# Optimization experiments

Hardware: AMD Instinct MI355X
Metric: run time of the kernel (lower is better)

Reference implementation:

```python
import jax, jax.numpy as jnp
import numpy as np

TEMPERATURE = 0.7
BIG_NEG = -1e30  # safe stand-in for -inf (keeps grads finite)


def setup_inputs() -> dict:
    key = jax.random.key(0)
    k1, k2, k3 = jax.random.split(key, 3)
    B, D = 8192, 256
    embeddings = jax.random.normal(k1, (B, D), dtype=jnp.float32)
    categories = jax.random.randint(k2, (B,), 0, 16, dtype=jnp.int64)
    font_labels = jax.random.randint(k3, (B,), 0, 2000, dtype=jnp.int64)
    return {"embeddings": embeddings, "categories": categories, "font_labels": font_labels}


def reference(embeddings, categories, font_labels):
    # L2-normalize rows
    e = embeddings / jnp.linalg.norm(embeddings, axis=1, keepdims=True)
    sims = jnp.matmul(e, e.T) / TEMPERATURE  # [B, B]
    B = sims.shape[0]

    same = categories[:, None] == categories[None, :]
    diag = jnp.eye(B, dtype=bool)
    pos_mask = same & ~diag           # same category, excluding self
    neg_mask = ~same                  # different category (self excluded implicitly)

    valid = pos_mask.any(axis=1) & neg_mask.any(axis=1)

    pos_sim = jnp.max(jnp.where(pos_mask, sims, BIG_NEG), axis=1)  # hardest positive per anchor
    neg_max = jnp.max(jnp.where(neg_mask, sims, BIG_NEG), axis=1)

    # logsumexp over {pos_sim} U neg_sims, numerically stable
    m = jnp.where(valid, jnp.maximum(pos_sim, neg_max), 0.0)
    pos_safe = jnp.where(valid, pos_sim, 0.0)
    exp_neg_sum = jnp.sum(jnp.where(neg_mask, jnp.exp(sims - m[:, None]), 0.0), axis=1)
    lse = m + jnp.log(jnp.exp(pos_safe - m) + exp_neg_sum)

    loss_per_anchor = -pos_safe + lse
    n_valid = jnp.maximum(jnp.sum(valid), 1)
    return jnp.sum(jnp.where(valid, loss_per_anchor, 0.0)) / n_valid
```

## Files before the change

kernel.cpp:

```cpp
#include <hip/hip_runtime.h>
#include <stdint.h>

#define NROWS 8192
#define DDIM 256
#define RB 128
#define NRB (NROWS / RB)
#define BN 32
#define NTILES (RB / BN)
#define NSLOT NRB

#define ESCALE 1.4356159f
#define LN2F   0.6931471806f
#define NEGBIG (-1e30f)

typedef __attribute__((ext_vector_type(8))) short short8;
typedef __attribute__((ext_vector_type(4))) float f32x4;

typedef __attribute__((address_space(3))) void lds_void;
typedef const __attribute__((address_space(1))) void gl_void;

__device__ __forceinline__ unsigned short f2bf(float x) {
  unsigned int u = __float_as_uint(x);
  u += 0x7fffu + ((u >> 16) & 1u);
  return (unsigned short)(u >> 16);
}

__global__ __launch_bounds__(256) void knorm(const float* __restrict__ emb,
                                             unsigned short* __restrict__ ebf) {
  const int wave = threadIdx.x >> 6, lane = threadIdx.x & 63;
  const int row = blockIdx.x * 4 + wave;
  const float4 v = *(const float4*)(emb + row * DDIM + lane * 4);
  float ss = v.x * v.x + v.y * v.y + v.z * v.z + v.w * v.w;
#pragma unroll
  for (int off = 1; off < 64; off <<= 1) ss += __shfl_xor(ss, off, 64);
  const float sc = rsqrtf(ss) * ESCALE;
  ushort4 o;
  o.x = f2bf(v.x * sc); o.y = f2bf(v.y * sc);
  o.z = f2bf(v.z * sc); o.w = f2bf(v.w * sc);
  *(ushort4*)(ebf + row * DDIM + lane * 4) = o;
}

__global__ __launch_bounds__(256) void kmain(const unsigned short* __restrict__ ebf,
                                             const int* __restrict__ cats,
                                             float* __restrict__ posP,
                                             float* __restrict__ sumP) {
  const int I = blockIdx.y, J = blockIdx.x;
  if (J < I) return;
  __shared__ alignas(16) unsigned short smem[2][BN * DDIM];
  __shared__ float cpm[4][RB], cns[4][RB];
  const int tid = threadIdx.x;
  const int lane = tid & 63, wave = tid >> 6;
  const int lane15 = lane & 15, quad = lane >> 4;
  const bool offd = (I != J);
  const int rowG = I * RB + wave * 32;
  const int col0 = J * RB;

  short8 a[2][8];
#pragma unroll
  for (int m = 0; m < 2; ++m)
#pragma unroll
    for (int kk = 0; kk < 8; ++kk)
      a[m][kk] = *(const short8*)(ebf + (rowG + m * 16 + lane15) * DDIM + kk * 32 + quad * 8);

  int cati[2][4];
#pragma unroll
  for (int m = 0; m < 2; ++m)
#pragma unroll
    for (int r = 0; r < 4; ++r)
      cati[m][r] = cats[rowG + m * 16 + quad * 4 + r];

  bool dlr[4];
#pragma unroll
  for (int r = 0; r < 4; ++r) dlr[r] = (lane15 == quad * 4 + r);

  float pm[2][4], ns[2][4];
#pragma unroll
  for (int m = 0; m < 2; ++m)
#pragma unroll
    for (int r = 0; r < 4; ++r) { pm[m][r] = NEGBIG; ns[m][r] = 0.f; }

#define STAGE(t, buf)                                                           \
  {                                                                             \
    const unsigned short* g = ebf +                                             \
        (size_t)(col0 + (t) * BN + (lane & 31)) * DDIM +                        \
        (wave * 2 + (lane >> 5)) * 8;                                           \
    char* lb = (char*)&smem[(buf)][0] + wave * 1024;                            \
    _Pragma("unroll")                                                           \
    for (int c = 0; c < 4; ++c)                                                 \
      __builtin_amdgcn_global_load_lds((gl_void*)(g + c * 64),                  \
                                       (lds_void*)(lb + c * 4096), 16, 0, 0);   \
  }

  STAGE(0, 0);

  for (int t = 0; t < NTILES; ++t) {
    __syncthreads();
    if (t + 1 < NTILES) STAGE(t + 1, (t + 1) & 1);
    const char* bb = (const char*)&smem[t & 1][0];
    const int colBase = col0 + t * BN;
    const int cjt[2] = {cats[colBase + lane15], cats[colBase + 16 + lane15]};

#pragma unroll
    for (int nt = 0; nt < 2; ++nt) {
      short8 b[8];
#pragma unroll
      for (int kk = 0; kk < 8; ++kk)
        b[kk] = *(const short8*)(bb + kk * 2048 + quad * 512 + nt * 256 + lane15 * 16);
      f32x4 acc0 = {0.f, 0.f, 0.f, 0.f}, acc1 = {0.f, 0.f, 0.f, 0.f};
      __builtin_amdgcn_s_setprio(1);
#pragma unroll
      for (int kk = 0; kk < 8; ++kk) {
        acc0 = __builtin_amdgcn_mfma_f32_16x16x32_bf16(a[0][kk], b[kk], acc0, 0, 0, 0);
        acc1 = __builtin_amdgcn_mfma_f32_16x16x32_bf16(a[1][kk], b[kk], acc1, 0, 0, 0);
      }
      __builtin_amdgcn_s_setprio(0);
      const int cj = cjt[nt];
      const bool dg0 = (rowG == colBase + nt * 16);
      const bool dg1 = (rowG + 16 == colBase + nt * 16);
      float cpmv = NEGBIG, cnsv = 0.f;
#pragma unroll
      for (int m = 0; m < 2; ++m) {
        const bool dg = m ? dg1 : dg0;
#pragma unroll
        for (int r = 0; r < 4; ++r) {
          const float s = m ? acc1[r] : acc0[r];
          const float e = __builtin_amdgcn_exp2f(s);
          const bool same = (cj == cati[m][r]);
          float psv = same ? s : NEGBIG;
          if (dg) psv = dlr[r] ? NEGBIG : psv;
          pm[m][r] = fmaxf(pm[m][r], psv);
          const float ev = same ? 0.f : e;
          ns[m][r] += ev;
          cpmv = fmaxf(cpmv, psv);
          cnsv += ev;
        }
      }
      if (offd) {
        cpmv = fmaxf(cpmv, __shfl_xor(cpmv, 16, 64)); cnsv += __shfl_xor(cnsv, 16, 64);
        cpmv = fmaxf(cpmv, __shfl_xor(cpmv, 32, 64)); cnsv += __shfl_xor(cnsv, 32, 64);
        if (quad == 0) {
          const int c = t * BN + nt * 16 + lane15;
          cpm[wave][c] = cpmv; cns[wave][c] = cnsv;
        }
      }
    }
  }

#pragma unroll
  for (int off = 1; off < 16; off <<= 1) {
#pragma unroll
    for (int m = 0; m < 2; ++m)
#pragma unroll
      for (int r = 0; r < 4; ++r) {
        pm[m][r] = fmaxf(pm[m][r], __shfl_xor(pm[m][r], off, 64));
        ns[m][r] += __shfl_xor(ns[m][r], off, 64);
      }
  }
  if (lane15 == 0) {
#pragma unroll
    for (int m = 0; m < 2; ++m)
#pragma unroll
      for (int r = 0; r < 4; ++r) {
        const int row = rowG + m * 16 + quad * 4 + r;
        posP[J * NROWS + row] = pm[m][r];
        sumP[J * NROWS + row] = ns[m][r];
      }
  }
  if (offd) {
    __syncthreads();
    if (tid < RB) {
      const float p = fmaxf(fmaxf(cpm[0][tid], cpm[1][tid]),
                            fmaxf(cpm[2][tid], cpm[3][tid]));
      const float n = cns[0][tid] + cns[1][tid] + cns[2][tid] + cns[3][tid];
      posP[I * NROWS + col0 + tid] = p;
      sumP[I * NROWS + col0 + tid] = n;
    }
  }
}

__global__ __launch_bounds__(256) void kmerge(const float* __restrict__ posP,
                                              const float* __restrict__ sumP,
                                              float* __restrict__ acc,
                                              float* __restrict__ out) {
  const int row = blockIdx.x * 256 + threadIdx.x;
  float pm = NEGBIG, ns = 0.f;
#pragma unroll 8
  for (int s = 0; s < NSLOT; ++s) {
    pm = fmaxf(pm, posP[s * NROWS + row]);
    ns += sumP[s * NROWS + row];
  }
  const bool valid = (pm > -1e29f) && (ns > 0.f);
  float loss = valid ? (logf(__builtin_amdgcn_exp2f(pm) + ns) - pm * LN2F) : 0.f;
  float cnt = valid ? 1.f : 0.f;
#pragma unroll
  for (int off = 1; off < 64; off <<= 1) {
    loss += __shfl_xor(loss, off, 64);
    cnt += __shfl_xor(cnt, off, 64);
  }
  if ((threadIdx.x & 63) == 0) {
    atomicAdd(&acc[0], loss);
    atomicAdd(&acc[1], cnt);
    __threadfence();
  }
  __syncthreads();
  if (threadIdx.x == 0) {
    const int prev = atomicAdd((int*)(acc + 2), 1);
    if (prev == (int)gridDim.x - 1) {
      const float L = atomicAdd(&acc[0], 0.f);
      const float C = atomicAdd(&acc[1], 0.f);
      out[0] = L / fmaxf(C, 1.f);
    }
  }
}

extern "C" void kernel_launch(void* const* d_in, const int* in_sizes, int n_in,
                              void* d_out, int out_size, void* d_ws, size_t ws_size,
                              hipStream_t stream) {
  const float* emb = (const float*)d_in[0];
  const int* cats = (const int*)d_in[1];
  float* out = (float*)d_out;

  char* ws = (char*)d_ws;
  float* accv = (float*)ws;
  unsigned short* ebf = (unsigned short*)(ws + 256);
  float* posP = (float*)(ws + 256 + NROWS * DDIM * 2);
  float* sumP = posP + NSLOT * NROWS;

  hipMemsetAsync(accv, 0, 16, stream);
  knorm<<<NROWS / 4, 256, 0, stream>>>(emb, ebf);
  kmain<<<dim3(NRB, NRB), 256, 0, stream>>>(ebf, cats, posP, sumP);
  kmerge<<<NROWS / 256, 256, 0, stream>>>(posP, sumP, accv, out);
}
```

Before: 141.2 us.

## Widen column span per block to 512 with triangular 1D grid and key-encoded partials

Each block now covers a 128-row strip against a 512-column span (16 tiles) instead of 128 columns, launched as a compact 1D triangular grid of 544 blocks. This replaces the 64x64 grid in which half the blocks exit immediately. The A fragment stays in registers across more tiles, and column-side partials are flushed per 128-column sub-block through double-buffered LDS. Partial maxima are stored as order-preserving unsigned keys, so the workspace can be zeroed inside knorm in place of a separate memset, and the merge reduces over 80 slots instead of 64. The risks are fewer, longer blocks, which hurts load balance on diagonal blocks, and more slot reads in the merge.

```diff
diff --git a/kernel.cpp b/kernel.cpp
--- a/kernel.cpp
+++ b/kernel.cpp
@@ -3,15 +3,22 @@
 
 #define NROWS 8192
 #define DDIM 256
-#define RB 128
-#define NRB (NROWS / RB)
 #define BN 32
-#define NTILES (RB / BN)
-#define NSLOT NRB
+#define NTILES 16
+#define BM 128
+#define NRB (NROWS / BM)
+#define NJ4 16
+#define NBLK 544
+#define NSLOT 80
 
 #define ESCALE 1.4356159f
 #define LN2F   0.6931471806f
 #define NEGBIG (-1e30f)
+
+#define WS_PMK   256
+#define WS_NS    (WS_PMK + NSLOT * NROWS * 4)
+#define WS_EBF   (WS_NS + NSLOT * NROWS * 4)
+#define WS_ZERO16 ((WS_EBF) / 16)
 
 typedef __attribute__((ext_vector_type(8))) short short8;
 typedef __attribute__((ext_vector_type(4))) float f32x4;
@@ -25,8 +32,20 @@
   return (unsigned short)(u >> 16);
 }
 
+__device__ __forceinline__ unsigned fkey(float f) {
+  unsigned b = __float_as_uint(f);
+  return (b & 0x80000000u) ? ~b : (b | 0x80000000u);
+}
+__device__ __forceinline__ float funkey(unsigned k) {
+  unsigned b = (k & 0x80000000u) ? (k & 0x7fffffffu) : ~k;
+  return __uint_as_float(b);
+}
+
 __global__ __launch_bounds__(256) void knorm(const float* __restrict__ emb,
-                                             unsigned short* __restrict__ ebf) {
+                                             unsigned short* __restrict__ ebf,
+                                             uint4* __restrict__ zbase) {
+  const int zi = blockIdx.x * 256 + threadIdx.x;
+  if (zi < WS_ZERO16) zbase[zi] = (uint4){0u, 0u, 0u, 0u};
   const int wave = threadIdx.x >> 6, lane = threadIdx.x & 63;
   const int row = blockIdx.x * 4 + wave;
   const float4 v = *(const float4*)(emb + row * DDIM + lane * 4);
@@ -42,18 +61,21 @@
 
 __global__ __launch_bounds__(256) void kmain(const unsigned short* __restrict__ ebf,
                                              const int* __restrict__ cats,
-                                             float* __restrict__ posP,
+                                             unsigned* __restrict__ posPk,
                                              float* __restrict__ sumP) {
-  const int I = blockIdx.y, J = blockIdx.x;
-  if (J < I) return;
+  int bid = blockIdx.x, I = 0, base = 0;
+  for (;; ++I) { const int c = NJ4 - (I >> 2); if (bid < base + c) break; base += c; }
+  const int J4 = (I >> 2) + (bid - base);
+  const int d = I - 4 * J4;
+  const int t0 = (d > 0) ? 4 * d : 0;
+
   __shared__ alignas(16) unsigned short smem[2][BN * DDIM];
-  __shared__ float cpm[4][RB], cns[4][RB];
+  __shared__ float cpm[2][4][BM], cns[2][4][BM];
   const int tid = threadIdx.x;
   const int lane = tid & 63, wave = tid >> 6;
   const int lane15 = lane & 15, quad = lane >> 4;
-  const bool offd = (I != J);
-  const int rowG = I * RB + wave * 32;
-  const int col0 = J * RB;
+  const int rowG = I * BM + wave * 32;
+  const int col0 = J4 * (NTILES * BN);
 
   short8 a[2][8];
 #pragma unroll
@@ -91,13 +113,27 @@
                                        (lds_void*)(lb + c * 4096), 16, 0, 0);   \
   }
 
-  STAGE(0, 0);
-
-  for (int t = 0; t < NTILES; ++t) {
+  STAGE(t0, t0 & 1);
+
+  for (int t = t0; t < NTILES; ++t) {
     __syncthreads();
+    if ((t & 3) == 0 && t > t0) {
+      const int jprev = 4 * J4 + (t >> 2) - 1;
+      if (jprev > I && tid < BM) {
+        const int pb = ((t >> 2) - 1) & 1;
+        const float p = fmaxf(fmaxf(cpm[pb][0][tid], cpm[pb][1][tid]),
+                              fmaxf(cpm[pb][2][tid], cpm[pb][3][tid]));
+        const float n = cns[pb][0][tid] + cns[pb][1][tid] +
+                        cns[pb][2][tid] + cns[pb][3][tid];
+        posPk[(NJ4 + I) * NROWS + jprev * BM + tid] = fkey(p);
+        sumP [(NJ4 + I) * NROWS + jprev * BM + tid] = n;
+      }
+    }
     if (t + 1 < NTILES) STAGE(t + 1, (t + 1) & 1);
     const char* bb = (const char*)&smem[t & 1][0];
     const int colBase = col0 + t * BN;
+    const int jt = colBase >> 7;
+    const bool colPath = (jt > I);
     const int cjt[2] = {cats[colBase + lane15], cats[colBase + 16 + lane15]};
 
 #pragma unroll
@@ -135,17 +171,30 @@
           cnsv += ev;
         }
       }
-      if (offd) {
+      if (colPath) {
         cpmv = fmaxf(cpmv, __shfl_xor(cpmv, 16, 64)); cnsv += __shfl_xor(cnsv, 16, 64);
         cpmv = fmaxf(cpmv, __shfl_xor(cpmv, 32, 64)); cnsv += __shfl_xor(cnsv, 32, 64);
         if (quad == 0) {
-          const int c = t * BN + nt * 16 + lane15;
-          cpm[wave][c] = cpmv; cns[wave][c] = cnsv;
+          const int cc = (colBase & 127) + nt * 16 + lane15;
+          const int pb = (t >> 2) & 1;
+          cpm[pb][wave][cc] = cpmv; cns[pb][wave][cc] = cnsv;
         }
       }
     }
   }
 
+  __syncthreads();
+  {
+    const int jlast = 4 * J4 + 3;
+    if (jlast > I && tid < BM) {
+      const float p = fmaxf(fmaxf(cpm[1][0][tid], cpm[1][1][tid]),
+                            fmaxf(cpm[1][2][tid], cpm[1][3][tid]));
+      const float n = cns[1][0][tid] + cns[1][1][tid] +
+                      cns[1][2][tid] + cns[1][3][tid];
+      posPk[(NJ4 + I) * NROWS + jlast * BM + tid] = fkey(p);
+      sumP [(NJ4 + I) * NROWS + jlast * BM + tid] = n;
+    }
+  }
 #pragma unroll
   for (int off = 1; off < 16; off <<= 1) {
 #pragma unroll
@@ -162,33 +211,24 @@
 #pragma unroll
       for (int r = 0; r < 4; ++r) {
         const int row = rowG + m * 16 + quad * 4 + r;
-        posP[J * NROWS + row] = pm[m][r];
-        sumP[J * NROWS + row] = ns[m][r];
-      }
-  }
-  if (offd) {
-    __syncthreads();
-    if (tid < RB) {
-      const float p = fmaxf(fmaxf(cpm[0][tid], cpm[1][tid]),
-                            fmaxf(cpm[2][tid], cpm[3][tid]));
-      const float n = cns[0][tid] + cns[1][tid] + cns[2][tid] + cns[3][tid];
-      posP[I * NROWS + col0 + tid] = p;
-      sumP[I * NROWS + col0 + tid] = n;
-    }
-  }
-}
-
-__global__ __launch_bounds__(256) void kmerge(const float* __restrict__ posP,
+        posPk[J4 * NROWS + row] = fkey(pm[m][r]);
+        sumP [J4 * NROWS + row] = ns[m][r];
+      }
+  }
+}
+
+__global__ __launch_bounds__(256) void kmerge(const unsigned* __restrict__ posPk,
                                               const float* __restrict__ sumP,
                                               float* __restrict__ acc,
                                               float* __restrict__ out) {
   const int row = blockIdx.x * 256 + threadIdx.x;
-  float pm = NEGBIG, ns = 0.f;
+  unsigned kmax = 0u; float ns = 0.f;
 #pragma unroll 8
   for (int s = 0; s < NSLOT; ++s) {
-    pm = fmaxf(pm, posP[s * NROWS + row]);
+    kmax = max(kmax, posPk[s * NROWS + row]);
     ns += sumP[s * NROWS + row];
   }
+  const float pm = funkey(kmax);
   const bool valid = (pm > -1e29f) && (ns > 0.f);
   float loss = valid ? (logf(__builtin_amdgcn_exp2f(pm) + ns) - pm * LN2F) : 0.f;
   float cnt = valid ? 1.f : 0.f;
@@ -222,12 +262,11 @@
 
   char* ws = (char*)d_ws;
   float* accv = (float*)ws;
-  unsigned short* ebf = (unsigned short*)(ws + 256);
-  float* posP = (float*)(ws + 256 + NROWS * DDIM * 2);
-  float* sumP = posP + NSLOT * NROWS;
-
-  hipMemsetAsync(accv, 0, 16, stream);
-  knorm<<<NROWS / 4, 256, 0, stream>>>(emb, ebf);
-  kmain<<<dim3(NRB, NRB), 256, 0, stream>>>(ebf, cats, posP, sumP);
-  kmerge<<<NROWS / 256, 256, 0, stream>>>(posP, sumP, accv, out);
-}
+  unsigned* posPk = (unsigned*)(ws + WS_PMK);
+  float* sumP = (float*)(ws + WS_NS);
+  unsigned short* ebf = (unsigned short*)(ws + WS_EBF);
+
+  knorm<<<NROWS / 4, 256, 0, stream>>>(emb, ebf, (uint4*)ws);
+  kmain<<<NBLK, 256, 0, stream>>>(ebf, cats, posPk, sumP);
+  kmerge<<<NROWS / 256, 256, 0, stream>>>(posPk, sumP, accv, out);
+}
```

New measurement: 130.2 us. -7.8%, faster.
